# Kernel optimization log

Hardware: AMD Instinct MI355X
Metric: run time of the kernel (lower is better)

## Reference

```python
import jax, jax.numpy as jnp
import numpy as np

S = 2048          # sequence length (single prefill sequence)
HID = 4096        # hidden_size
NH, NKV, HD = 32, 8, 128   # q heads, kv heads, head_dim
THETA = 10000.0
SCALE = HD ** -0.5


def setup_inputs() -> dict:
    key = jax.random.key(0)
    k1, k2, k3 = jax.random.split(key, 3)
    hidden_states = jax.random.normal(k1, (S, HID), jnp.float32)
    positions = jnp.arange(S, dtype=jnp.int32)
    W_qkv = jax.random.normal(k2, (HID, (NH + 2 * NKV) * HD), jnp.float32) * 0.02
    W_o = jax.random.normal(k3, (NH * HD, HID), jnp.float32) * 0.02
    return {"hidden_states": hidden_states, "positions": positions,
            "W_qkv": W_qkv, "W_o": W_o}


def _rope(x, positions):
    # x: [T, H, HD]; neox-style RoPE (rotate halves, is_neox_style=True)
    half = HD // 2
    inv_freq = 1.0 / (THETA ** (jnp.arange(half, dtype=jnp.float32) / half))
    freqs = positions.astype(jnp.float32)[:, None] * inv_freq[None, :]  # [T, half]
    cos = jnp.cos(freqs)[:, None, :]
    sin = jnp.sin(freqs)[:, None, :]
    x1, x2 = x[..., :half], x[..., half:]
    return jnp.concatenate([x1 * cos - x2 * sin, x2 * cos + x1 * sin], axis=-1)


def reference(hidden_states, positions, W_qkv, W_o):
    # fused QKV projection then split (q_size = NH*HD, kv_size = NKV*HD)
    qkv = hidden_states @ W_qkv                      # [S, (NH+2*NKV)*HD]
    q, k, v = jnp.split(qkv, [NH * HD, NH * HD + NKV * HD], axis=1)
    q = _rope(q.reshape(S, NH, HD), positions)       # [S, NH, HD]
    k = _rope(k.reshape(S, NKV, HD), positions)      # [S, NKV, HD]
    v = v.reshape(S, NKV, HD)
    # GQA: broadcast kv heads to query heads
    rep = NH // NKV
    k = jnp.repeat(k, rep, axis=1)                   # [S, NH, HD]
    v = jnp.repeat(v, rep, axis=1)
    scores = jnp.einsum('qhd,khd->hqk', q, k) * SCALE  # [NH, S, S]
    causal = jnp.tril(jnp.ones((S, S), dtype=bool))
    scores = jnp.where(causal[None], scores, jnp.finfo(scores.dtype).min)
    attn = jax.nn.softmax(scores, axis=-1)
    out = jnp.einsum('hqk,khd->qhd', attn, v).reshape(S, NH * HD)
    return out @ W_o                                 # [S, HID]
```

## Files before the change

### kernel.cpp

```cpp
#include <hip/hip_runtime.h>
#include <math.h>
#include <stdint.h>

#define S_LEN 2048
#define HID 4096
#define NH 32
#define NKV 8
#define HD 128
#define QKV_N ((NH + 2*NKV) * HD)
#define NQK (NH + NKV)
static __device__ __constant__ const float SCALE_F = 0.08838834764831845f;

typedef __bf16 bf16x8 __attribute__((ext_vector_type(8)));
typedef __bf16 bf16x4 __attribute__((ext_vector_type(4)));
typedef float  f32x4  __attribute__((ext_vector_type(4)));
typedef uint32_t u32x4 __attribute__((ext_vector_type(4)));

#define GLD_LDS(gptr, lptr) \
  __builtin_amdgcn_global_load_lds( \
      (const __attribute__((address_space(1))) uint32_t*)(gptr), \
      (__attribute__((address_space(3))) uint32_t*)(lptr), 16, 0, 0)

__global__ void cast_bf16_kernel(const float4* __restrict__ in, __bf16* __restrict__ out, int n4) {
  int i = blockIdx.x * blockDim.x + threadIdx.x;
  if (i >= n4) return;
  float4 v = in[i];
  bf16x4 o = { (__bf16)v.x, (__bf16)v.y, (__bf16)v.z, (__bf16)v.w };
  *(bf16x4*)(out + (size_t)i * 4) = o;
}

__global__ void transpose_cast_kernel(const float* __restrict__ in, __bf16* __restrict__ out,
                                      int R, int C) {
  __shared__ float tile[32][33];
  int bx = blockIdx.x * 32;
  int by = blockIdx.y * 32;
  int tx = threadIdx.x, ty = threadIdx.y;
  for (int i = 0; i < 32; i += 8)
    tile[ty + i][tx] = in[(size_t)(by + ty + i) * C + bx + tx];
  __syncthreads();
  for (int i = 0; i < 32; i += 8)
    out[(size_t)(bx + ty + i) * R + by + tx] = (__bf16)tile[tx][ty + i];
}

__global__ void transpose_v_kernel(const __bf16* __restrict__ qkv, __bf16* __restrict__ Vt) {
  __shared__ __bf16 tile[32][33];
  int kvh = blockIdx.z;
  int sb = blockIdx.x * 32;
  int db = blockIdx.y * 32;
  int tx = threadIdx.x, ty = threadIdx.y;
  const __bf16* src = qkv + (size_t)(NH + NKV) * HD + (size_t)kvh * HD;
  for (int i = 0; i < 32; i += 8)
    tile[ty + i][tx] = src[(size_t)(sb + ty + i) * QKV_N + db + tx];
  __syncthreads();
  for (int i = 0; i < 32; i += 8)
    Vt[((size_t)kvh * HD + db + ty + i) * S_LEN + sb + tx] = tile[tx][ty + i];
}

__global__ void rope_kernel(const __bf16* __restrict__ qkv, const int* __restrict__ pos,
                            __bf16* __restrict__ Qr, __bf16* __restrict__ Kr) {
  int idx = blockIdx.x * blockDim.x + threadIdx.x;
  int half = idx & 63;
  int t = idx >> 6;
  int hh = t % NQK;
  int s = t / NQK;
  if (s >= S_LEN) return;
  float p = (float)pos[s];
  float inv_freq = exp2f((float)half * -0.2076205059304601f);
  float ang = p * inv_freq;
  float cs = cosf(ang), sn = sinf(ang);
  const __bf16* src; __bf16* dst;
  if (hh < NH) {
    src = qkv + (size_t)s * QKV_N + (size_t)hh * HD;
    dst = Qr + ((size_t)s * NH + hh) * HD;
  } else {
    int kh = hh - NH;
    src = qkv + (size_t)s * QKV_N + (size_t)NH * HD + (size_t)kh * HD;
    dst = Kr + ((size_t)s * NKV + kh) * HD;
  }
  float x1 = (float)src[half], x2 = (float)src[half + 64];
  dst[half]      = (__bf16)(x1 * cs - x2 * sn);
  dst[half + 64] = (__bf16)(x2 * cs + x1 * sn);
}

template <typename OutT>
__global__ __launch_bounds__(512, 2) void gemm8p_kernel(const __bf16* __restrict__ A,
                                                        const __bf16* __restrict__ Bt,
                                                        OutT* __restrict__ C,
                                                        int M, int N, int K) {
  __shared__ __align__(16) __bf16 sA[2][2][256 * 32];
  __shared__ __align__(16) __bf16 sB[2][2][256 * 32];
  const int tid = threadIdx.x;
  const int lane = tid & 63;
  const int wave = tid >> 6;
  const int quad = lane >> 4;
  const int l16 = lane & 15;
  const int wm = (wave >> 2) * 128;
  const int wn = (wave & 3) * 64;

  const int nx = gridDim.x;
  size_t bm, bn;
  if (gridDim.y == 8 && (nx & 7) == 0) {
    int lin = blockIdx.y * nx + blockIdx.x;
    int j = lin >> 3, xcd = lin & 7;
    bm = (size_t)(j & 7) * 256;
    bn = (size_t)(xcd * (nx >> 3) + (j >> 3)) * 256;
  } else {
    bm = (size_t)blockIdx.y * 256;
    bn = (size_t)blockIdx.x * 256;
  }

  const int NT = K >> 6;
  const int rsw = (l16 >> 1) & 3;

  f32x4 acc[8][4] = {};
  bf16x8 aR[2][4], bR[2][4];

  const int row0 = tid >> 2;
  const int chL = (tid & 3) ^ ((tid >> 3) & 3);
  const uint64_t off128 = (uint64_t)128 * K * 2;
  uint64_t aGA = (uint64_t)(uintptr_t)A + ((bm + row0) * (size_t)K) * 2 + (size_t)chL * 16;
  uint64_t bGA = (uint64_t)(uintptr_t)Bt + ((bn + row0) * (size_t)K) * 2 + (size_t)chL * 16;

  typedef __attribute__((address_space(3))) __bf16 lds_bf16;
  const uint32_t sAb = (uint32_t)(uintptr_t)(lds_bf16*)&sA[0][0][0];
  const uint32_t sBb = (uint32_t)(uintptr_t)(lds_bf16*)&sB[0][0][0];
  const uint32_t wlds = (uint32_t)__builtin_amdgcn_readfirstlane(wave * 1024);
  const uint32_t aBase = sAb + (uint32_t)(((wm + l16) * 32 + (quad ^ rsw) * 8) * 2);
  const uint32_t bBase = sBb + (uint32_t)(((wn + l16) * 32 + (quad ^ rsw) * 8) * 2);

#define LDSA(bf, kk) (sAb + (bf) * 32768u + (kk) * 16384u)
#define LDSB(bf, kk) (sBb + (bf) * 32768u + (kk) * 16384u)

#define STAGE_ASM(ga, ldsbase) \
  asm volatile("s_mov_b32 m0, %0\n\t" \
               "global_load_lds_dwordx4 %2, off\n\t" \
               "s_mov_b32 m0, %1\n\t" \
               "global_load_lds_dwordx4 %3, off" \
               :: "s"((ldsbase) + wlds), "s"((ldsbase) + wlds + 8192u), \
                  "v"(ga), "v"((ga) + off128) : "memory")

#define DSRD4(dst, baseaddr) do {                                                 \
    u32x4 t0_, t1_, t2_, t3_;                                                     \
    asm volatile("ds_read_b128 %0, %4\n\t"                                        \
                 "ds_read_b128 %1, %4 offset:1024\n\t"                            \
                 "ds_read_b128 %2, %4 offset:2048\n\t"                            \
                 "ds_read_b128 %3, %4 offset:3072"                                \
                 : "=&v"(t0_), "=&v"(t1_), "=&v"(t2_), "=&v"(t3_)                 \
                 : "v"(baseaddr));                                                \
    dst[0] = __builtin_bit_cast(bf16x8, t0_);                                     \
    dst[1] = __builtin_bit_cast(bf16x8, t1_);                                     \
    dst[2] = __builtin_bit_cast(bf16x8, t2_);                                     \
    dst[3] = __builtin_bit_cast(bf16x8, t3_);                                     \
  } while (0)

#define ISSUE_A(set, bf, kk, ih) DSRD4(aR[set], aBase + (bf) * 32768u + (kk) * 16384u + (ih) * 4096u)
#define ISSUE_B(set, bf, kk)     DSRD4(bR[set], bBase + (bf) * 32768u + (kk) * 16384u)

#define MFMA16(as, bs, ih) do {                                                   \
    __builtin_amdgcn_s_setprio(1);                                                \
    _Pragma("unroll")                                                             \
    for (int i_ = 0; i_ < 4; ++i_)                                                \
      _Pragma("unroll")                                                           \
      for (int j_ = 0; j_ < 4; ++j_)                                              \
        acc[(ih) * 4 + i_][j_] = __builtin_amdgcn_mfma_f32_16x16x32_bf16(         \
            aR[as][i_], bR[bs][j_], acc[(ih) * 4 + i_][j_], 0, 0, 0);             \
    __builtin_amdgcn_s_setprio(0);                                                \
    __builtin_amdgcn_sched_barrier(0);                                            \
  } while (0)

#define BAR() __builtin_amdgcn_s_barrier()
#define LGKM4() do { asm volatile("s_waitcnt lgkmcnt(4)");                        \
                     __builtin_amdgcn_sched_barrier(0); } while (0)
#define LGKM8() do { asm volatile("s_waitcnt lgkmcnt(8)");                        \
                     __builtin_amdgcn_sched_barrier(0); } while (0)
#define VMCNT4() do { asm volatile("s_waitcnt vmcnt(4)");                         \
                      __builtin_amdgcn_sched_barrier(0); } while (0)

  STAGE_ASM(aGA,        LDSA(0, 0));
  STAGE_ASM(bGA,        LDSB(0, 0));
  STAGE_ASM(aGA + 64,   LDSA(0, 1));
  STAGE_ASM(bGA + 64,   LDSB(0, 1));
  STAGE_ASM(aGA + 128,  LDSA(1, 0));
  STAGE_ASM(bGA + 128,  LDSB(1, 0));
  aGA += 192; bGA += 192;
  asm volatile("s_waitcnt vmcnt(8)");
  __builtin_amdgcn_sched_barrier(0);
  BAR();
  ISSUE_A(0, 0, 0, 0); ISSUE_B(0, 0, 0);

  for (int u = 0; u < (NT >> 1); ++u) {
    VMCNT4();
    ISSUE_A(1, 0, 0, 1);
    BAR();
    LGKM4();
    MFMA16(0, 0, 0);
    STAGE_ASM(aGA, LDSA(1, 1)); aGA += 64;
    ISSUE_A(0, 0, 1, 0); ISSUE_B(1, 0, 1);
    BAR();
    LGKM8();
    MFMA16(1, 0, 1);
    STAGE_ASM(bGA, LDSB(1, 1)); bGA += 64;
    VMCNT4();
    ISSUE_A(1, 0, 1, 1);
    BAR();
    LGKM4();
    MFMA16(0, 1, 0);
    STAGE_ASM(aGA, LDSA(0, 0)); aGA += 64;
    ISSUE_A(0, 1, 0, 0); ISSUE_B(0, 1, 0);
    BAR();
    LGKM8();
    MFMA16(1, 1, 1);
    STAGE_ASM(bGA, LDSB(0, 0)); bGA += 64;
    VMCNT4();
    ISSUE_A(1, 1, 0, 1);
    BAR();
    LGKM4();
    MFMA16(0, 0, 0);
    STAGE_ASM(aGA, LDSA(0, 1)); aGA += 64;
    ISSUE_A(0, 1, 1, 0); ISSUE_B(1, 1, 1);
    BAR();
    LGKM8();
    MFMA16(1, 0, 1);
    STAGE_ASM(bGA, LDSB(0, 1)); bGA += 64;
    VMCNT4();
    ISSUE_A(1, 1, 1, 1);
    BAR();
    LGKM4();
    MFMA16(0, 1, 0);
    STAGE_ASM(aGA, LDSA(1, 0)); aGA += 64;
    ISSUE_A(0, 0, 0, 0); ISSUE_B(0, 0, 0);
    BAR();
    LGKM8();
    MFMA16(1, 1, 1);
    STAGE_ASM(bGA, LDSB(1, 0)); bGA += 64;
  }

  asm volatile("s_waitcnt vmcnt(0) lgkmcnt(0)");
  __builtin_amdgcn_sched_barrier(0);

  #pragma unroll
  for (int i = 0; i < 8; ++i)
    #pragma unroll
    for (int j = 0; j < 4; ++j)
      #pragma unroll
      for (int r = 0; r < 4; ++r) {
        size_t row = bm + wm + i * 16 + quad * 4 + r;
        size_t col = bn + wn + j * 16 + l16;
        C[row * (size_t)N + col] = (OutT)acc[i][j][r];
      }

#undef LDSA
#undef LDSB
#undef STAGE_ASM
#undef DSRD4
#undef ISSUE_A
#undef ISSUE_B
#undef MFMA16
#undef BAR
#undef LGKM4
#undef LGKM8
#undef VMCNT4
}

__global__ __launch_bounds__(256, 2) void attn_kernel(const __bf16* __restrict__ Qr,
                                                      const __bf16* __restrict__ Kr,
                                                      const __bf16* __restrict__ Vt,
                                                      __bf16* __restrict__ O) {
  __shared__ __align__(16) char smem[73728];
  __bf16* Ps = (__bf16*)(smem + 65536);

  const int bid = blockIdx.x;
  const int h = bid & (NH - 1);
  const int qb = (S_LEN / 64 - 1) - (bid >> 5);
  const int kvh = h >> 2;
  const int tid = threadIdx.x;
  const int lane = tid & 63, wave = tid >> 6;
  const int quad = lane >> 4, l16 = lane & 15;
  const int sw = l16 & 7;
  const int q0 = qb * 64;

#define STAGE_KV(kbase, bufv) do {                                                 \
    char* kd_ = smem + (bufv) * 16384;                                             \
    char* vd_ = smem + 32768 + (bufv) * 16384;                                     \
    _Pragma("unroll")                                                              \
    for (int pass_ = 0; pass_ < 4; ++pass_) {                                      \
      int c_ = pass_ * 256 + tid;                                                  \
      int row_ = c_ >> 4, ch_ = c_ & 15;                                           \
      int chs_ = ch_ ^ (row_ & 7);                                                 \
      GLD_LDS(&Kr[(size_t)((kbase) + row_) * (NKV * HD) + (size_t)kvh * HD + chs_ * 8], \
              kd_ + c_ * 16);                                                      \
    }                                                                              \
    _Pragma("unroll")                                                              \
    for (int pass_ = 0; pass_ < 4; ++pass_) {                                      \
      int c_ = pass_ * 256 + tid;                                                  \
      int d_ = c_ >> 3, ch_ = c_ & 7;                                              \
      int chs_ = ch_ ^ (d_ & 7);                                                   \
      GLD_LDS(&Vt[((size_t)kvh * HD + d_) * S_LEN + (kbase) + chs_ * 8],           \
              vd_ + c_ * 16);                                                      \
    }                                                                              \
  } while (0)

  bf16x8 qf[4];
  {
    const __bf16* qp = Qr + (size_t)(q0 + wave * 16 + l16) * (NH * HD) + (size_t)h * HD + quad * 8;
    for (int kk = 0; kk < 4; ++kk) qf[kk] = *(const bf16x8*)(qp + kk * 32);
  }
  f32x4 oacc[8] = {};
  float m2 = -INFINITY, l_i = 0.0f;
  const float C2 = SCALE_F * 1.4426950408889634f;

  int buf = 0;
  STAGE_KV(0, 0);
  for (int kb = 0; kb <= q0; kb += 64) {
    __syncthreads();
    if (kb + 64 <= q0) STAGE_KV(kb + 64, buf ^ 1);

    const __bf16* Ks = (const __bf16*)(smem + buf * 16384);
    const __bf16* Vs = (const __bf16*)(smem + 32768 + buf * 16384);

    f32x4 sc[4] = {};
    __builtin_amdgcn_s_setprio(1);
    for (int jt = 0; jt < 4; ++jt)
      for (int kk = 0; kk < 4; ++kk) {
        bf16x8 kf = *(const bf16x8*)&Ks[(jt * 16 + l16) * 128 + ((kk * 4 + quad) ^ sw) * 8];
        sc[jt] = __builtin_amdgcn_mfma_f32_16x16x32_bf16(kf, qf[kk], sc[jt], 0, 0, 0);
      }
    __builtin_amdgcn_s_setprio(0);

    float s[16];
    for (int jt = 0; jt < 4; ++jt)
      for (int r = 0; r < 4; ++r) s[jt * 4 + r] = sc[jt][r];
    if (kb == q0) {
      int qloc = wave * 16 + l16;
      for (int jt = 0; jt < 4; ++jt)
        for (int r = 0; r < 4; ++r)
          if (jt * 16 + quad * 4 + r > qloc) s[jt * 4 + r] = -INFINITY;
    }
    float mx = s[0];
    for (int i = 1; i < 16; ++i) mx = fmaxf(mx, s[i]);
    mx = fmaxf(mx, __shfl_xor(mx, 16, 64));
    mx = fmaxf(mx, __shfl_xor(mx, 32, 64));
    float m2new = fmaxf(m2, mx * C2);
    float alpha = exp2f(m2 - m2new);
    float pv[16], sum = 0.0f;
    for (int i = 0; i < 16; ++i) { pv[i] = exp2f(fmaf(s[i], C2, -m2new)); sum += pv[i]; }
    sum += __shfl_xor(sum, 16, 64);
    sum += __shfl_xor(sum, 32, 64);
    l_i = l_i * alpha + sum;
    m2 = m2new;
    for (int dt = 0; dt < 8; ++dt) oacc[dt] *= alpha;

    __bf16* pw = Ps + wave * 1024 + l16 * 64;
    for (int jt = 0; jt < 4; ++jt) {
      bf16x4 pk = { (__bf16)pv[jt*4+0], (__bf16)pv[jt*4+1], (__bf16)pv[jt*4+2], (__bf16)pv[jt*4+3] };
      int chunk = jt * 2 + (quad >> 1);
      *(bf16x4*)&pw[((chunk ^ sw) * 8) + (quad & 1) * 4] = pk;
    }
    __builtin_amdgcn_s_setprio(1);
    for (int half = 0; half < 2; ++half) {
      bf16x8 pf = *(const bf16x8*)&pw[((half * 4 + quad) ^ sw) * 8];
      for (int dt = 0; dt < 8; ++dt) {
        bf16x8 vf = *(const bf16x8*)&Vs[(dt * 16 + l16) * 64 + ((half * 4 + quad) ^ sw) * 8];
        oacc[dt] = __builtin_amdgcn_mfma_f32_16x16x32_bf16(vf, pf, oacc[dt], 0, 0, 0);
      }
    }
    __builtin_amdgcn_s_setprio(0);
    buf ^= 1;
  }
  __syncthreads();

#undef STAGE_KV

  float* scr = (float*)smem + wave * 2112;
  float inv = 1.0f / l_i;
  for (int dt = 0; dt < 8; ++dt) {
    f32x4 v = oacc[dt] * inv;
    *(f32x4*)&scr[l16 * 132 + dt * 16 + quad * 4] = v;
  }
  for (int it = 0; it < 4; ++it) {
    int c = it * 64 + lane;
    int row = c >> 4, ch = c & 15;
    const float* sp = &scr[row * 132 + ch * 8];
    f32x4 a = *(const f32x4*)sp;
    f32x4 b = *(const f32x4*)(sp + 4);
    bf16x8 o = { (__bf16)a[0], (__bf16)a[1], (__bf16)a[2], (__bf16)a[3],
                 (__bf16)b[0], (__bf16)b[1], (__bf16)b[2], (__bf16)b[3] };
    *(bf16x8*)&O[(size_t)(q0 + wave * 16 + row) * (NH * HD) + (size_t)h * HD + ch * 8] = o;
  }
}

extern "C" void kernel_launch(void* const* d_in, const int* in_sizes, int n_in,
                              void* d_out, int out_size, void* d_ws, size_t ws_size,
                              hipStream_t stream) {
  const float* hidden    = (const float*)d_in[0];
  const int*   positions = (const int*)d_in[1];
  const float* Wqkv      = (const float*)d_in[2];
  const float* Wo        = (const float*)d_in[3];
  float* out = (float*)d_out;

  char* p = (char*)d_ws;
  auto alloc = [&](size_t bytes) { char* r = p; p += (bytes + 255) & ~(size_t)255; return r; };
  __bf16* hid_bf = (__bf16*)alloc((size_t)S_LEN * HID * 2);
  __bf16* wqkvT  = (__bf16*)alloc((size_t)QKV_N * HID * 2);
  __bf16* woT    = (__bf16*)alloc((size_t)HID * HID * 2);
  __bf16* qkv    = (__bf16*)alloc((size_t)S_LEN * QKV_N * 2);
  __bf16* Qr     = (__bf16*)alloc((size_t)S_LEN * NH * HD * 2);
  __bf16* Kr     = (__bf16*)alloc((size_t)S_LEN * NKV * HD * 2);
  __bf16* Vt     = (__bf16*)alloc((size_t)S_LEN * NKV * HD * 2);
  __bf16* attn   = hid_bf;

  {
    int n4 = S_LEN * HID / 4;
    cast_bf16_kernel<<<(n4 + 255) / 256, 256, 0, stream>>>((const float4*)hidden, hid_bf, n4);
  }
  transpose_cast_kernel<<<dim3(QKV_N / 32, HID / 32), dim3(32, 8), 0, stream>>>(Wqkv, wqkvT, HID, QKV_N);
  transpose_cast_kernel<<<dim3(HID / 32, HID / 32), dim3(32, 8), 0, stream>>>(Wo, woT, HID, HID);
  gemm8p_kernel<__bf16><<<dim3(QKV_N / 256, S_LEN / 256), 512, 0, stream>>>(
      hid_bf, wqkvT, qkv, S_LEN, QKV_N, HID);
  {
    int total = S_LEN * NQK * 64;
    rope_kernel<<<total / 256, 256, 0, stream>>>(qkv, positions, Qr, Kr);
  }
  transpose_v_kernel<<<dim3(S_LEN / 32, HD / 32, NKV), dim3(32, 8), 0, stream>>>(qkv, Vt);
  attn_kernel<<<NH * (S_LEN / 64), 256, 0, stream>>>(Qr, Kr, Vt, attn);
  gemm8p_kernel<float><<<dim3(HID / 256, S_LEN / 256), 512, 0, stream>>>(
      attn, woT, out, S_LEN, HID, HID);
}
```

Before: 496.9 us.

## Split-K the output projection GEMM in two with a separate reduction kernel

The output projection GEMM now runs with split-K of 2 along a grid z dimension. Each half writes fp32 partials into reused workspace buffers (the wqkvT and qkv regions), and a new elementwise kernel adds the two partials into the output. This doubles the block count from 128 to 256 so the GPU's compute units are better filled. The cost is an extra 32 MB fp32 partial write plus read and one more kernel launch.

```diff
diff --git a/kernel.cpp b/kernel.cpp
--- a/kernel.cpp
+++ b/kernel.cpp
@@ -27,6 +27,17 @@
   float4 v = in[i];
   bf16x4 o = { (__bf16)v.x, (__bf16)v.y, (__bf16)v.z, (__bf16)v.w };
   *(bf16x4*)(out + (size_t)i * 4) = o;
+}
+
+__global__ void add_f32_kernel(const float4* __restrict__ a, const float4* __restrict__ b,
+                               float4* __restrict__ o, int n4) {
+  int i = blockIdx.x * blockDim.x + threadIdx.x;
+  int stride = gridDim.x * blockDim.x;
+  for (; i < n4; i += stride) {
+    float4 x = a[i], y = b[i];
+    float4 r; r.x = x.x + y.x; r.y = x.y + y.y; r.z = x.z + y.z; r.w = x.w + y.w;
+    o[i] = r;
+  }
 }
 
 __global__ void transpose_cast_kernel(const float* __restrict__ in, __bf16* __restrict__ out,
@@ -85,8 +96,9 @@
 template <typename OutT>
 __global__ __launch_bounds__(512, 2) void gemm8p_kernel(const __bf16* __restrict__ A,
                                                         const __bf16* __restrict__ Bt,
-                                                        OutT* __restrict__ C,
-                                                        int M, int N, int K) {
+                                                        OutT* __restrict__ C0,
+                                                        OutT* __restrict__ C1,
+                                                        int M, int N, int Kext, int ld) {
   __shared__ __align__(16) __bf16 sA[2][2][256 * 32];
   __shared__ __align__(16) __bf16 sB[2][2][256 * 32];
   const int tid = threadIdx.x;
@@ -96,6 +108,11 @@
   const int l16 = lane & 15;
   const int wm = (wave >> 2) * 128;
   const int wn = (wave & 3) * 64;
+
+  const int z = blockIdx.z;
+  A += (size_t)z * Kext;
+  Bt += (size_t)z * Kext;
+  OutT* __restrict__ C = z ? C1 : C0;
 
   const int nx = gridDim.x;
   size_t bm, bn;
@@ -109,7 +126,7 @@
     bn = (size_t)blockIdx.x * 256;
   }
 
-  const int NT = K >> 6;
+  const int NT = Kext >> 6;
   const int rsw = (l16 >> 1) & 3;
 
   f32x4 acc[8][4] = {};
@@ -117,9 +134,9 @@
 
   const int row0 = tid >> 2;
   const int chL = (tid & 3) ^ ((tid >> 3) & 3);
-  const uint64_t off128 = (uint64_t)128 * K * 2;
-  uint64_t aGA = (uint64_t)(uintptr_t)A + ((bm + row0) * (size_t)K) * 2 + (size_t)chL * 16;
-  uint64_t bGA = (uint64_t)(uintptr_t)Bt + ((bn + row0) * (size_t)K) * 2 + (size_t)chL * 16;
+  const uint64_t off128 = (uint64_t)128 * ld * 2;
+  uint64_t aGA = (uint64_t)(uintptr_t)A + ((bm + row0) * (size_t)ld) * 2 + (size_t)chL * 16;
+  uint64_t bGA = (uint64_t)(uintptr_t)Bt + ((bn + row0) * (size_t)ld) * 2 + (size_t)chL * 16;
 
   typedef __attribute__((address_space(3))) __bf16 lds_bf16;
   const uint32_t sAb = (uint32_t)(uintptr_t)(lds_bf16*)&sA[0][0][0];
@@ -409,20 +426,28 @@
   __bf16* Vt     = (__bf16*)alloc((size_t)S_LEN * NKV * HD * 2);
   __bf16* attn   = hid_bf;
 
+  float* Cp0 = (float*)wqkvT;
+  float* Cp1 = (float*)qkv;
+
   {
     int n4 = S_LEN * HID / 4;
     cast_bf16_kernel<<<(n4 + 255) / 256, 256, 0, stream>>>((const float4*)hidden, hid_bf, n4);
   }
   transpose_cast_kernel<<<dim3(QKV_N / 32, HID / 32), dim3(32, 8), 0, stream>>>(Wqkv, wqkvT, HID, QKV_N);
   transpose_cast_kernel<<<dim3(HID / 32, HID / 32), dim3(32, 8), 0, stream>>>(Wo, woT, HID, HID);
-  gemm8p_kernel<__bf16><<<dim3(QKV_N / 256, S_LEN / 256), 512, 0, stream>>>(
-      hid_bf, wqkvT, qkv, S_LEN, QKV_N, HID);
+  gemm8p_kernel<__bf16><<<dim3(QKV_N / 256, S_LEN / 256, 1), 512, 0, stream>>>(
+      hid_bf, wqkvT, qkv, qkv, S_LEN, QKV_N, HID, HID);
   {
     int total = S_LEN * NQK * 64;
     rope_kernel<<<total / 256, 256, 0, stream>>>(qkv, positions, Qr, Kr);
   }
   transpose_v_kernel<<<dim3(S_LEN / 32, HD / 32, NKV), dim3(32, 8), 0, stream>>>(qkv, Vt);
   attn_kernel<<<NH * (S_LEN / 64), 256, 0, stream>>>(Qr, Kr, Vt, attn);
-  gemm8p_kernel<float><<<dim3(HID / 256, S_LEN / 256), 512, 0, stream>>>(
-      attn, woT, out, S_LEN, HID, HID);
-}
+  gemm8p_kernel<float><<<dim3(HID / 256, S_LEN / 256, 2), 512, 0, stream>>>(
+      attn, woT, Cp0, Cp1, S_LEN, HID, HID / 2, HID);
+  {
+    int n4 = S_LEN * HID / 4;
+    add_f32_kernel<<<2048, 256, 0, stream>>>((const float4*)Cp0, (const float4*)Cp1,
+                                             (float4*)out, n4);
+  }
+}
```

Result: no change. 505.0 us (+1.6%).
